# Optimization experiments

Hardware: AMD Instinct MI355X
Metric: run time of the kernel (lower is better)

## Reference

```python
import jax, jax.numpy as jnp
import numpy as np

HIDDEN = 512
INPUT = 128
OUTPUT = 128
PRED_LEN = 32


def _gru_cell(h, gi, gh):
    # gi, gh: [B, 3H] pre-activations (input-side and hidden-side)
    i_r, i_z, i_n = jnp.split(gi, 3, axis=-1)
    h_r, h_z, h_n = jnp.split(gh, 3, axis=-1)
    r = jax.nn.sigmoid(i_r + h_r)
    z = jax.nn.sigmoid(i_z + h_z)
    n = jnp.tanh(i_n + r * h_n)
    return (1.0 - z) * n + z * h


def setup_inputs() -> dict:
    key = jax.random.key(0)
    ks = jax.random.split(key, 7)
    B, L = 512, 512
    s = 0.05
    return {
        "z_seq": jax.random.normal(ks[0], (B, L, INPUT), dtype=jnp.float32),
        "W_ih": jax.random.normal(ks[1], (3 * HIDDEN, INPUT), dtype=jnp.float32) * s,
        "W_hh": jax.random.normal(ks[2], (3 * HIDDEN, HIDDEN), dtype=jnp.float32) * s,
        "b_ih": jax.random.normal(ks[3], (3 * HIDDEN,), dtype=jnp.float32) * s,
        "b_hh": jax.random.normal(ks[4], (3 * HIDDEN,), dtype=jnp.float32) * s,
        "W_out": jax.random.normal(ks[5], (OUTPUT, HIDDEN), dtype=jnp.float32) * s,
        "b_out": jax.random.normal(ks[6], (OUTPUT,), dtype=jnp.float32) * s,
    }


def reference(z_seq, W_ih, W_hh, b_ih, b_hh, W_out, b_out):
    B, L, C = z_seq.shape
    h0 = jnp.zeros((B, HIDDEN), dtype=z_seq.dtype)

    # Precompute input-side pre-activations for all encode steps: [L, B, 3H]
    gi_enc = jnp.einsum('blc,gc->lbg', z_seq, W_ih) + b_ih

    def enc_step(h, gi):
        gh = h @ W_hh.T + b_hh
        return _gru_cell(h, gi, gh), None

    h_t, _ = jax.lax.scan(enc_step, h0, gi_enc)

    # Decode: input is always zeros, so input-side pre-activation is just b_ih
    gi_dec = jnp.broadcast_to(b_ih, (B, 3 * HIDDEN))

    def dec_step(h, _):
        gh = h @ W_hh.T + b_hh
        h_new = _gru_cell(h, gi_dec, gh)
        y = h_new @ W_out.T + b_out
        return h_new, y

    _, ys = jax.lax.scan(dec_step, h_t, None, length=PRED_LEN)  # [pred_len, B, O]
    return jnp.transpose(ys, (1, 0, 2))  # [B, pred_len, O]
```

## Files before the change

kernel.cpp:

```cpp
#include <hip/hip_runtime.h>

#define BATCH 512
#define SEQL  512
#define NIN   128
#define NH    512
#define NOUT  128
#define PRED  32
#define NSTEP (SEQL + PRED)

#define G_B 8
#define G_H 32
#define BT  64
#define NWG (G_B * G_H)
#define NTHREADS 256

#define OFF_WIH  24576
#define OFF_WOUT 30720
#define OFF_TR   38912
#define LDS_SH   40448

typedef short bf16x8 __attribute__((ext_vector_type(8)));
typedef float f32x4 __attribute__((ext_vector_type(4)));
typedef unsigned int u32x4 __attribute__((ext_vector_type(4)));

#define MFMA __builtin_amdgcn_mfma_f32_16x16x32_bf16

__device__ __forceinline__ unsigned short f2bf(float f) {
    unsigned int u = __float_as_uint(f);
    u = (u + 0x7fffu + ((u >> 16) & 1u)) >> 16;
    return (unsigned short)u;
}
__device__ __forceinline__ float sigm(float x) {
    x = fminf(fmaxf(x, -30.f), 30.f);
    return 1.f / (1.f + __expf(-x));
}
__device__ __forceinline__ float tanh_f(float x) {
    x = fminf(fmaxf(x, -15.f), 15.f);
    float e = __expf(2.f * x);
    return (e - 1.f) / (e + 1.f);
}

__global__ __launch_bounds__(256) void zero_kernel(unsigned short* hbuf, int* cnt)
{
    const int tid = threadIdx.x, wg = blockIdx.x;
    u32x4 z = {0, 0, 0, 0};
    char* base = (char*)hbuf + ((wg * 256 + tid) * 32);
    asm volatile("global_store_dwordx4 %0, %1, off sc1" :: "v"(base), "v"(z) : "memory");
    asm volatile("global_store_dwordx4 %0, %1, off offset:16 sc1" :: "v"(base), "v"(z) : "memory");
    if (wg == 0) {
        int zz = 0;
        asm volatile("global_store_dword %0, %1, off sc1" :: "v"(cnt + tid), "v"(zz) : "memory");
        asm volatile("global_store_dword %0, %1, off sc1" :: "v"(cnt + 256 + tid), "v"(zz) : "memory");
        asm volatile("global_store_dword %0, %1, off sc1" :: "v"(cnt + 512 + tid), "v"(zz) : "memory");
        asm volatile("global_store_dword %0, %1, off sc1" :: "v"(cnt + 768 + tid), "v"(zz) : "memory");
    }
}

__global__ __launch_bounds__(NTHREADS, 1) void gru_kernel(
    const float* __restrict__ z_seq, const float* __restrict__ W_ih,
    const float* __restrict__ W_hh, const float* __restrict__ b_ih,
    const float* __restrict__ b_hh, const float* __restrict__ W_out,
    const float* __restrict__ b_out, float* __restrict__ out,
    unsigned short* __restrict__ hbuf, int* __restrict__ cnt)
{
    __shared__ unsigned short s_w[LDS_SH];
    const int tid = threadIdx.x;
    const int wg  = blockIdx.x;
    const int bg  = wg & 7;
    const int hs  = wg >> 3;

    for (int i = tid; i < 24576; i += NTHREADS) {
        int e = i & 7, ln = (i >> 3) & 63, ks = (i >> 9) & 15, g = i >> 13;
        int unit = hs * 16 + (ln & 15);
        int k = ks * 32 + (ln >> 4) * 8 + e;
        s_w[i] = f2bf(W_hh[(g * 512 + unit) * 512 + k]);
    }
    for (int i = tid; i < 6144; i += NTHREADS) {
        int e = i & 7, ln = (i >> 3) & 63, ks = (i >> 9) & 3, g = i >> 11;
        int unit = hs * 16 + (ln & 15);
        int k = ks * 32 + (ln >> 4) * 8 + e;
        s_w[OFF_WIH + i] = f2bf(W_ih[(g * 512 + unit) * 128 + k]);
    }
    for (int i = tid; i < 8192; i += NTHREADS) {
        int e = i & 7, ln = (i >> 3) & 63, ks = i >> 9;
        int ocol = hs * 4 + (ln & 3);
        int k = ks * 32 + (ln >> 4) * 8 + e;
        s_w[OFF_WOUT + i] = f2bf(W_out[ocol * 512 + k]);
    }
    __syncthreads();

    const int lane = tid & 63;
    const int wave = tid >> 6;
    const int li   = lane & 15;
    const int kq   = lane >> 4;
    const int jg   = hs * 16 + li;

    const float bihr = b_ih[jg], bihz = b_ih[NH + jg], bihn = b_ih[2 * NH + jg];
    const float bhhr = b_hh[jg], bhhz = b_hh[NH + jg], bhhn = b_hh[2 * NH + jg];
    const float bo   = b_out[hs * 4 + (li & 3)];

    const int aRow = bg * BT + wave * 16 + li;
    const int cRow = bg * BT + wave * 16 + kq * 4;
    float hreg[4] = {0.f, 0.f, 0.f, 0.f};

    const unsigned short* fb = s_w + lane * 8;
    unsigned short* tr = s_w + OFF_TR + wave * 384;

    int* myFlag = cnt + ((bg * 4 + wave) << 5) + hs;
    const int* fp = cnt + ((bg * 4 + wave) << 5) + (lane & 31);
    int  dead  = 0;

    f32x4 ir = {0,0,0,0}, iz = {0,0,0,0}, in = {0,0,0,0};
    {
        const float* zrow = z_seq + ((long)aRow * SEQL + 0) * NIN + kq * 8;
#pragma unroll
        for (int ks = 0; ks < 4; ++ks) {
            float4 z0 = *(const float4*)(zrow + ks * 32);
            float4 z1 = *(const float4*)(zrow + ks * 32 + 4);
            union { bf16x8 v; unsigned short u[8]; } az;
            az.u[0] = f2bf(z0.x); az.u[1] = f2bf(z0.y);
            az.u[2] = f2bf(z0.z); az.u[3] = f2bf(z0.w);
            az.u[4] = f2bf(z1.x); az.u[5] = f2bf(z1.y);
            az.u[6] = f2bf(z1.z); az.u[7] = f2bf(z1.w);
            ir = MFMA(az.v, *(const bf16x8*)(fb + OFF_WIH + ks * 512), ir, 0, 0, 0);
            iz = MFMA(az.v, *(const bf16x8*)(fb + OFF_WIH + 2048 + ks * 512), iz, 0, 0, 0);
            in = MFMA(az.v, *(const bf16x8*)(fb + OFF_WIH + 4096 + ks * 512), in, 0, 0, 0);
        }
    }

    for (int t = 0; t <= NSTEP; ++t) {
        const unsigned short* hin  = hbuf + (t & 1) * (BATCH * NH);
        unsigned short*       hout = hbuf + ((t & 1) ^ 1) * (BATCH * NH);

        const unsigned short* hrow = hin + aRow * NH + kq * 8;
        bf16x8 a[16];
#pragma unroll
        for (int ks = 0; ks < 16; ++ks)
            asm volatile("global_load_dwordx4 %0, %1, off offset:%2 sc1"
                         : "=v"(a[ks]) : "v"(hrow), "i"(ks * 64) : "memory");
        asm volatile("s_waitcnt vmcnt(0)" ::: "memory");
        __builtin_amdgcn_sched_barrier(0);

        if (t > SEQL) {
            int td = t - SEQL - 1;
            f32x4 y4 = {0, 0, 0, 0};
#pragma unroll
            for (int ks = 0; ks < 16; ++ks)
                y4 = MFMA(a[ks], *(const bf16x8*)(fb + OFF_WOUT + ks * 512), y4, 0, 0, 0);
            if (li < 4) {
#pragma unroll
                for (int q = 0; q < 4; ++q)
                    out[((long)(cRow + q) * PRED + td) * NOUT + hs * 4 + li] = y4[q] + bo;
            }
        }
        if (t == NSTEP) break;

        f32x4 hr = {0,0,0,0}, hz = {0,0,0,0}, hn = {0,0,0,0};
#pragma unroll
        for (int ks = 0; ks < 16; ++ks) {
            hr = MFMA(a[ks], *(const bf16x8*)(fb + ks * 512), hr, 0, 0, 0);
            hz = MFMA(a[ks], *(const bf16x8*)(fb + 8192 + ks * 512), hz, 0, 0, 0);
            hn = MFMA(a[ks], *(const bf16x8*)(fb + 16384 + ks * 512), hn, 0, 0, 0);
        }

#pragma unroll
        for (int q = 0; q < 4; ++q) {
            float r  = sigm(bihr + ir[q] + bhhr + hr[q]);
            float zz = sigm(bihz + iz[q] + bhhz + hz[q]);
            float nn = tanh_f(bihn + in[q] + r * (bhhn + hn[q]));
            float hq = (1.f - zz) * nn + zz * hreg[q];
            hreg[q]  = hq;
            tr[(kq * 4 + q) * 24 + li] = f2bf(hq);
        }
        asm volatile("s_waitcnt lgkmcnt(0)" ::: "memory");
        __builtin_amdgcn_sched_barrier(0);

        if (lane < 32) {
            bf16x8 hv = *(const bf16x8*)(tr + (lane >> 1) * 24 + (lane & 1) * 8);
            int grow = bg * BT + wave * 16 + (lane >> 1);
            unsigned short* hp = hout + grow * NH + hs * 16 + (lane & 1) * 8;
            asm volatile("global_store_dwordx4 %0, %1, off sc1"
                         :: "v"(hp), "v"(hv) : "memory");
        }
        asm volatile("s_waitcnt vmcnt(0)" ::: "memory");
        if (lane == 0) {
            int v = t + 1;
            asm volatile("global_store_dword %0, %1, off sc1"
                         :: "v"(myFlag), "v"(v) : "memory");
        }

        f32x4 nir = {0,0,0,0}, niz = {0,0,0,0}, nin = {0,0,0,0};
        if (t + 1 < SEQL) {
            const float* zrow = z_seq + ((long)aRow * SEQL + (t + 1)) * NIN + kq * 8;
#pragma unroll
            for (int ks = 0; ks < 4; ++ks) {
                float4 z0 = *(const float4*)(zrow + ks * 32);
                float4 z1 = *(const float4*)(zrow + ks * 32 + 4);
                union { bf16x8 v; unsigned short u[8]; } az;
                az.u[0] = f2bf(z0.x); az.u[1] = f2bf(z0.y);
                az.u[2] = f2bf(z0.z); az.u[3] = f2bf(z0.w);
                az.u[4] = f2bf(z1.x); az.u[5] = f2bf(z1.y);
                az.u[6] = f2bf(z1.z); az.u[7] = f2bf(z1.w);
                nir = MFMA(az.v, *(const bf16x8*)(fb + OFF_WIH + ks * 512), nir, 0, 0, 0);
                niz = MFMA(az.v, *(const bf16x8*)(fb + OFF_WIH + 2048 + ks * 512), niz, 0, 0, 0);
                nin = MFMA(az.v, *(const bf16x8*)(fb + OFF_WIH + 4096 + ks * 512), nin, 0, 0, 0);
            }
        }

        const int target = t + 1;
        if (!dead) {
            int patience = 1000000;
            for (;;) {
                int f;
                asm volatile("global_load_dword %0, %1, off sc1\n\ts_waitcnt vmcnt(0)"
                             : "=v"(f) : "v"(fp) : "memory");
                if (__ballot(f >= target) == ~0ull) break;
                if (--patience == 0) { dead = 1; break; }
            }
        }
        __builtin_amdgcn_sched_barrier(0);

        ir = nir; iz = niz; in = nin;
    }
}

extern "C" void kernel_launch(void* const* d_in, const int* in_sizes, int n_in,
                              void* d_out, int out_size, void* d_ws, size_t ws_size,
                              hipStream_t stream)
{
    const float* z_seq = (const float*)d_in[0];
    const float* W_ih  = (const float*)d_in[1];
    const float* W_hh  = (const float*)d_in[2];
    const float* b_ih  = (const float*)d_in[3];
    const float* b_hh  = (const float*)d_in[4];
    const float* W_out = (const float*)d_in[5];
    const float* b_out = (const float*)d_in[6];
    float* out = (float*)d_out;

    unsigned short* hbuf = (unsigned short*)d_ws;
    int* cnt = (int*)((char*)d_ws + (size_t)2 * BATCH * NH * 2);

    zero_kernel<<<dim3(64), dim3(256), 0, stream>>>(hbuf, cnt);
    gru_kernel<<<dim3(NWG), dim3(NTHREADS), 0, stream>>>(
        z_seq, W_ih, W_hh, b_ih, b_hh, W_out, b_out, out, hbuf, cnt);
}
```

Measured before the change: 3.204 ms.

## Add runtime-verified fast sync path with non-sc1 h loads and per-WG flags

Replaces the per-wave flag barrier with one flag per workgroup (after a __syncthreads), polled by a single lane that reads a whole row of flags with vector loads. At startup it checks that all workgroups of a batch group sit on the same XCD and runs a coherence probe. If both checks pass, a fast path loads h and polls flags without sc1, using buffer_inv instead. It also skips the h load at t=0 and shrinks the zero kernel. The aim is to cut the cross-workgroup synchronisation and coherent-load latency that dominates each recurrent step. The cost is a fragile startup handshake, and correctness depends on the XCD placement check.

```diff
diff --git a/kernel.cpp b/kernel.cpp
--- a/kernel.cpp
+++ b/kernel.cpp
@@ -19,11 +19,20 @@
 #define OFF_TR   38912
 #define LDS_SH   40448
 
+#define SLOW_FLAG_OFF 1048576
+#define XCD_OFF       1052672
+#define CANT_OFF      1053696
+#define CANC_OFF      1054720
+#define FAST_FLAG_OFF 1056768
+#define WS_NEED       1058816
+
 typedef short bf16x8 __attribute__((ext_vector_type(8)));
 typedef float f32x4 __attribute__((ext_vector_type(4)));
 typedef unsigned int u32x4 __attribute__((ext_vector_type(4)));
 
 #define MFMA __builtin_amdgcn_mfma_f32_16x16x32_bf16
+
+template<bool B> struct BC { static constexpr bool value = B; };
 
 __device__ __forceinline__ unsigned short f2bf(float f) {
     unsigned int u = __float_as_uint(f);
@@ -39,20 +48,62 @@
     float e = __expf(2.f * x);
     return (e - 1.f) / (e + 1.f);
 }
-
-__global__ __launch_bounds__(256) void zero_kernel(unsigned short* hbuf, int* cnt)
+__device__ __forceinline__ int poll_word_sc1(const int* p) {
+    int v;
+    asm volatile("global_load_dword %0, %1, off sc1\n\ts_waitcnt vmcnt(0)"
+                 : "=v"(v) : "v"(p) : "memory");
+    return v;
+}
+
+#define POLL_ROW_BODY(PREFIX, SCBITS)                                      \
+    int4 f0, f1, f2, f3, f4, f5, f6, f7;                                   \
+    asm volatile(                                                          \
+        PREFIX                                                             \
+        "global_load_dwordx4 %0, %8, off " SCBITS "\n\t"                   \
+        "global_load_dwordx4 %1, %8, off offset:16 " SCBITS "\n\t"         \
+        "global_load_dwordx4 %2, %8, off offset:32 " SCBITS "\n\t"         \
+        "global_load_dwordx4 %3, %8, off offset:48 " SCBITS "\n\t"         \
+        "global_load_dwordx4 %4, %8, off offset:64 " SCBITS "\n\t"         \
+        "global_load_dwordx4 %5, %8, off offset:80 " SCBITS "\n\t"         \
+        "global_load_dwordx4 %6, %8, off offset:96 " SCBITS "\n\t"         \
+        "global_load_dwordx4 %7, %8, off offset:112 " SCBITS "\n\t"        \
+        "s_waitcnt vmcnt(0)"                                               \
+        : "=&v"(f0), "=&v"(f1), "=&v"(f2), "=&v"(f3),                      \
+          "=&v"(f4), "=&v"(f5), "=&v"(f6), "=&v"(f7)                       \
+        : "v"(p) : "memory");                                              \
+    int mn = min(min(min(min(f0.x, f0.y), min(f0.z, f0.w)),                \
+                     min(min(f1.x, f1.y), min(f1.z, f1.w))),               \
+                 min(min(min(f2.x, f2.y), min(f2.z, f2.w)),                \
+                     min(min(f3.x, f3.y), min(f3.z, f3.w))));              \
+    mn = min(mn, min(min(min(min(f4.x, f4.y), min(f4.z, f4.w)),            \
+                         min(min(f5.x, f5.y), min(f5.z, f5.w))),           \
+                     min(min(min(f6.x, f6.y), min(f6.z, f6.w)),            \
+                         min(min(f7.x, f7.y), min(f7.z, f7.w)))));         \
+    int mx = max(max(max(max(f0.x, f0.y), max(f0.z, f0.w)),                \
+                     max(max(f1.x, f1.y), max(f1.z, f1.w))),               \
+                 max(max(max(f2.x, f2.y), max(f2.z, f2.w)),                \
+                     max(max(f3.x, f3.y), max(f3.z, f3.w))));              \
+    mx = max(mx, max(max(max(max(f4.x, f4.y), max(f4.z, f4.w)),            \
+                         max(max(f5.x, f5.y), max(f5.z, f5.w))),           \
+                     max(max(max(f6.x, f6.y), max(f6.z, f6.w)),            \
+                         max(max(f7.x, f7.y), max(f7.z, f7.w)))));         \
+    return make_int2(mn, mx);
+
+__device__ __forceinline__ int2 poll_row_sc1(const int* p) { POLL_ROW_BODY("", "sc1") }
+__device__ __forceinline__ int2 poll_row_inv(const int* p) {
+    POLL_ROW_BODY("buffer_inv\n\ts_waitcnt vmcnt(0)\n\t", "")
+}
+
+__global__ __launch_bounds__(256) void zero_kernel(char* ws)
 {
     const int tid = threadIdx.x, wg = blockIdx.x;
     u32x4 z = {0, 0, 0, 0};
-    char* base = (char*)hbuf + ((wg * 256 + tid) * 32);
-    asm volatile("global_store_dwordx4 %0, %1, off sc1" :: "v"(base), "v"(z) : "memory");
-    asm volatile("global_store_dwordx4 %0, %1, off offset:16 sc1" :: "v"(base), "v"(z) : "memory");
     if (wg == 0) {
-        int zz = 0;
-        asm volatile("global_store_dword %0, %1, off sc1" :: "v"(cnt + tid), "v"(zz) : "memory");
-        asm volatile("global_store_dword %0, %1, off sc1" :: "v"(cnt + 256 + tid), "v"(zz) : "memory");
-        asm volatile("global_store_dword %0, %1, off sc1" :: "v"(cnt + 512 + tid), "v"(zz) : "memory");
-        asm volatile("global_store_dword %0, %1, off sc1" :: "v"(cnt + 768 + tid), "v"(zz) : "memory");
+        char* p = ws + SLOW_FLAG_OFF + tid * 16;
+        asm volatile("global_store_dwordx4 %0, %1, off sc1" :: "v"(p), "v"(z) : "memory");
+    } else if (tid < 192) {
+        char* p = ws + XCD_OFF + tid * 16;
+        asm volatile("global_store_dwordx4 %0, %1, off sc1" :: "v"(p), "v"(z) : "memory");
     }
 }
 
@@ -61,13 +112,21 @@
     const float* __restrict__ W_hh, const float* __restrict__ b_ih,
     const float* __restrict__ b_hh, const float* __restrict__ W_out,
     const float* __restrict__ b_out, float* __restrict__ out,
-    unsigned short* __restrict__ hbuf, int* __restrict__ cnt)
+    char* __restrict__ ws, int allow_fast)
 {
     __shared__ unsigned short s_w[LDS_SH];
+    __shared__ int s_fast;
     const int tid = threadIdx.x;
     const int wg  = blockIdx.x;
     const int bg  = wg & 7;
     const int hs  = wg >> 3;
+
+    unsigned short* hbuf = (unsigned short*)ws;
+    int* sfl  = (int*)(ws + SLOW_FLAG_OFF) + bg * 64;
+    int* ffl  = (int*)(ws + FAST_FLAG_OFF) + bg * 64;
+    int* xrow = (int*)(ws + XCD_OFF)  + bg * 32;
+    int* T    = (int*)(ws + CANT_OFF) + bg * 32;
+    int* C    = (int*)(ws + CANC_OFF) + bg * 32;
 
     for (int i = tid; i < 24576; i += NTHREADS) {
         int e = i & 7, ln = (i >> 3) & 63, ks = (i >> 9) & 15, g = i >> 13;
@@ -87,7 +146,69 @@
         int k = ks * 32 + (ln >> 4) * 8 + e;
         s_w[OFF_WOUT + i] = f2bf(W_out[ocol * 512 + k]);
     }
+
+    unsigned xcd;
+    asm volatile("s_getreg_b32 %0, hwreg(20, 0, 32)" : "=s"(xcd));
+    xcd &= 255u;
+    if (tid == 0) {
+        int z0 = 0;
+        asm volatile("global_store_dword %0, %1, off sc1" :: "v"(ffl + hs), "v"(z0) : "memory");
+        asm volatile("s_waitcnt vmcnt(0)" ::: "memory");
+        int xv = (int)xcd + 1;
+        asm volatile("global_store_dword %0, %1, off sc1" :: "v"(xrow + hs), "v"(xv) : "memory");
+
+        if (hs == 0) {
+            unsigned long long tm;
+            asm volatile("s_memtime %0" : "=s"(tm));
+            int m1 = (int)((unsigned)tm | 1u);
+            asm volatile("global_store_dword %0, %1, off sc1" :: "v"(T), "v"(m1) : "memory");
+            asm volatile("s_waitcnt vmcnt(0)" ::: "memory");
+            asm volatile("global_store_dword %0, %1, off sc1" :: "v"(C), "v"(m1) : "memory");
+            int p = 1000000;
+            while (poll_word_sc1(C + 1) == 0 && --p) {}
+            if (p) {
+                int m2 = m1 ^ 0x5A5A5A5A;
+                asm volatile("global_store_dword %0, %1, off sc1" :: "v"(T), "v"(m2) : "memory");
+                asm volatile("s_waitcnt vmcnt(0)" ::: "memory");
+                int one = 1;
+                asm volatile("global_store_dword %0, %1, off sc1" :: "v"(C + 2), "v"(one) : "memory");
+            }
+        } else if (hs == 1) {
+            int p = 1000000, m1;
+            while ((m1 = poll_word_sc1(C)) == 0 && --p) {}
+            int verdict = 1;
+            if (p) {
+                int pv;
+                asm volatile("global_load_dword %0, %1, off\n\ts_waitcnt vmcnt(0)"
+                             : "=v"(pv) : "v"(T) : "memory");
+                asm volatile("" :: "v"(pv));
+                int one = 1;
+                asm volatile("global_store_dword %0, %1, off sc1" :: "v"(C + 1), "v"(one) : "memory");
+                int q = 1000000;
+                while (poll_word_sc1(C + 2) == 0 && --q) {}
+                if (q) {
+                    int v2;
+                    asm volatile("buffer_inv\n\ts_waitcnt vmcnt(0)\n\t"
+                                 "global_load_dword %0, %1, off\n\ts_waitcnt vmcnt(0)"
+                                 : "=v"(v2) : "v"(T) : "memory");
+                    verdict = (v2 == (m1 ^ 0x5A5A5A5A)) ? 2 : 1;
+                }
+            }
+            asm volatile("global_store_dword %0, %1, off sc1" :: "v"(C + 3), "v"(verdict) : "memory");
+        }
+
+        int ok = 0, p2 = 1000000;
+        for (;;) {
+            int2 mm = poll_row_sc1(xrow);
+            if (mm.x > 0) { ok = (mm.x == mm.y); break; }
+            if (--p2 == 0) break;
+        }
+        int vd = 0, p3 = 1000000;
+        while ((vd = poll_word_sc1(C + 3)) == 0 && --p3) {}
+        s_fast = (allow_fast && ok && vd == 2) ? 1 : 0;
+    }
     __syncthreads();
+    const bool fast = (s_fast != 0);
 
     const int lane = tid & 63;
     const int wave = tid >> 6;
@@ -105,10 +226,7 @@
 
     const unsigned short* fb = s_w + lane * 8;
     unsigned short* tr = s_w + OFF_TR + wave * 384;
-
-    int* myFlag = cnt + ((bg * 4 + wave) << 5) + hs;
-    const int* fp = cnt + ((bg * 4 + wave) << 5) + (lane & 31);
-    int  dead  = 0;
+    int dead = 0;
 
     f32x4 ir = {0,0,0,0}, iz = {0,0,0,0}, in = {0,0,0,0};
     {
@@ -128,100 +246,121 @@
         }
     }
 
-    for (int t = 0; t <= NSTEP; ++t) {
-        const unsigned short* hin  = hbuf + (t & 1) * (BATCH * NH);
-        unsigned short*       hout = hbuf + ((t & 1) ^ 1) * (BATCH * NH);
-
-        const unsigned short* hrow = hin + aRow * NH + kq * 8;
-        bf16x8 a[16];
-#pragma unroll
-        for (int ks = 0; ks < 16; ++ks)
-            asm volatile("global_load_dwordx4 %0, %1, off offset:%2 sc1"
-                         : "=v"(a[ks]) : "v"(hrow), "i"(ks * 64) : "memory");
-        asm volatile("s_waitcnt vmcnt(0)" ::: "memory");
-        __builtin_amdgcn_sched_barrier(0);
-
-        if (t > SEQL) {
-            int td = t - SEQL - 1;
-            f32x4 y4 = {0, 0, 0, 0};
-#pragma unroll
-            for (int ks = 0; ks < 16; ++ks)
-                y4 = MFMA(a[ks], *(const bf16x8*)(fb + OFF_WOUT + ks * 512), y4, 0, 0, 0);
-            if (li < 4) {
-#pragma unroll
-                for (int q = 0; q < 4; ++q)
-                    out[((long)(cRow + q) * PRED + td) * NOUT + hs * 4 + li] = y4[q] + bo;
-            }
+    auto body = [&](auto FC) {
+        constexpr bool FAST = decltype(FC)::value;
+        for (int t = 0; t <= NSTEP; ++t) {
+            const unsigned short* hin  = hbuf + (t & 1) * (BATCH * NH);
+            unsigned short*       hout = hbuf + ((t & 1) ^ 1) * (BATCH * NH);
+
+            bf16x8 a[16];
+            if (t == 0) {
+                bf16x8 az = {0,0,0,0,0,0,0,0};
+#pragma unroll
+                for (int ks = 0; ks < 16; ++ks) a[ks] = az;
+            } else {
+                const unsigned short* hrow = hin + aRow * NH + kq * 8;
+#pragma unroll
+                for (int ks = 0; ks < 16; ++ks) {
+                    if constexpr (FAST)
+                        asm volatile("global_load_dwordx4 %0, %1, off offset:%2"
+                                     : "=v"(a[ks]) : "v"(hrow), "i"(ks * 64) : "memory");
+                    else
+                        asm volatile("global_load_dwordx4 %0, %1, off offset:%2 sc1"
+                                     : "=v"(a[ks]) : "v"(hrow), "i"(ks * 64) : "memory");
+                }
+                asm volatile("s_waitcnt vmcnt(0)" ::: "memory");
+                __builtin_amdgcn_sched_barrier(0);
+            }
+
+            if (t > SEQL) {
+                int td = t - SEQL - 1;
+                f32x4 y4 = {0, 0, 0, 0};
+#pragma unroll
+                for (int ks = 0; ks < 16; ++ks)
+                    y4 = MFMA(a[ks], *(const bf16x8*)(fb + OFF_WOUT + ks * 512), y4, 0, 0, 0);
+                if (li < 4) {
+#pragma unroll
+                    for (int q = 0; q < 4; ++q)
+                        out[((long)(cRow + q) * PRED + td) * NOUT + hs * 4 + li] = y4[q] + bo;
+                }
+            }
+            if (t == NSTEP) break;
+
+            f32x4 hr = {0,0,0,0}, hz = {0,0,0,0}, hn = {0,0,0,0};
+#pragma unroll
+            for (int ks = 0; ks < 16; ++ks) {
+                hr = MFMA(a[ks], *(const bf16x8*)(fb + ks * 512), hr, 0, 0, 0);
+                hz = MFMA(a[ks], *(const bf16x8*)(fb + 8192 + ks * 512), hz, 0, 0, 0);
+                hn = MFMA(a[ks], *(const bf16x8*)(fb + 16384 + ks * 512), hn, 0, 0, 0);
+            }
+
+#pragma unroll
+            for (int q = 0; q < 4; ++q) {
+                float r  = sigm(bihr + ir[q] + bhhr + hr[q]);
+                float zz = sigm(bihz + iz[q] + bhhz + hz[q]);
+                float nn = tanh_f(bihn + in[q] + r * (bhhn + hn[q]));
+                float hq = (1.f - zz) * nn + zz * hreg[q];
+                hreg[q]  = hq;
+                tr[(kq * 4 + q) * 24 + li] = f2bf(hq);
+            }
+            asm volatile("s_waitcnt lgkmcnt(0)" ::: "memory");
+            __builtin_amdgcn_sched_barrier(0);
+
+            if (lane < 32) {
+                bf16x8 hv = *(const bf16x8*)(tr + (lane >> 1) * 24 + (lane & 1) * 8);
+                int grow = bg * BT + wave * 16 + (lane >> 1);
+                unsigned short* hp = hout + grow * NH + hs * 16 + (lane & 1) * 8;
+                asm volatile("global_store_dwordx4 %0, %1, off sc1"
+                             :: "v"(hp), "v"(hv) : "memory");
+            }
+            asm volatile("s_waitcnt vmcnt(0)" ::: "memory");
+            __syncthreads();
+            if (tid == 0) {
+                int v = t + 1;
+                asm volatile("global_store_dword %0, %1, off sc1"
+                             :: "v"(sfl + hs), "v"(v) : "memory");
+                asm volatile("global_store_dword %0, %1, off sc1"
+                             :: "v"(ffl + hs), "v"(v) : "memory");
+            }
+
+            f32x4 nir = {0,0,0,0}, niz = {0,0,0,0}, nin = {0,0,0,0};
+            if (t + 1 < SEQL) {
+                const float* zrow = z_seq + ((long)aRow * SEQL + (t + 1)) * NIN + kq * 8;
+#pragma unroll
+                for (int ks = 0; ks < 4; ++ks) {
+                    float4 z0 = *(const float4*)(zrow + ks * 32);
+                    float4 z1 = *(const float4*)(zrow + ks * 32 + 4);
+                    union { bf16x8 v; unsigned short u[8]; } az;
+                    az.u[0] = f2bf(z0.x); az.u[1] = f2bf(z0.y);
+                    az.u[2] = f2bf(z0.z); az.u[3] = f2bf(z0.w);
+                    az.u[4] = f2bf(z1.x); az.u[5] = f2bf(z1.y);
+                    az.u[6] = f2bf(z1.z); az.u[7] = f2bf(z1.w);
+                    nir = MFMA(az.v, *(const bf16x8*)(fb + OFF_WIH + ks * 512), nir, 0, 0, 0);
+                    niz = MFMA(az.v, *(const bf16x8*)(fb + OFF_WIH + 2048 + ks * 512), niz, 0, 0, 0);
+                    nin = MFMA(az.v, *(const bf16x8*)(fb + OFF_WIH + 4096 + ks * 512), nin, 0, 0, 0);
+                }
+            }
+
+            const int target = t + 1;
+            int bail = 0;
+            if (!dead && lane == 0) {
+                int patience = 1000000;
+                for (;;) {
+                    int2 mm;
+                    if constexpr (FAST) mm = poll_row_inv(ffl);
+                    else                mm = poll_row_sc1(sfl);
+                    if (mm.x >= target) break;
+                    if (--patience == 0) { bail = 1; break; }
+                }
+            }
+            dead |= __builtin_amdgcn_readfirstlane(bail);
+            __builtin_amdgcn_sched_barrier(0);
+
+            ir = nir; iz = niz; in = nin;
         }
-        if (t == NSTEP) break;
-
-        f32x4 hr = {0,0,0,0}, hz = {0,0,0,0}, hn = {0,0,0,0};
-#pragma unroll
-        for (int ks = 0; ks < 16; ++ks) {
-            hr = MFMA(a[ks], *(const bf16x8*)(fb + ks * 512), hr, 0, 0, 0);
-            hz = MFMA(a[ks], *(const bf16x8*)(fb + 8192 + ks * 512), hz, 0, 0, 0);
-            hn = MFMA(a[ks], *(const bf16x8*)(fb + 16384 + ks * 512), hn, 0, 0, 0);
-        }
-
-#pragma unroll
-        for (int q = 0; q < 4; ++q) {
-            float r  = sigm(bihr + ir[q] + bhhr + hr[q]);
-            float zz = sigm(bihz + iz[q] + bhhz + hz[q]);
-            float nn = tanh_f(bihn + in[q] + r * (bhhn + hn[q]));
-            float hq = (1.f - zz) * nn + zz * hreg[q];
-            hreg[q]  = hq;
-            tr[(kq * 4 + q) * 24 + li] = f2bf(hq);
-        }
-        asm volatile("s_waitcnt lgkmcnt(0)" ::: "memory");
-        __builtin_amdgcn_sched_barrier(0);
-
-        if (lane < 32) {
-            bf16x8 hv = *(const bf16x8*)(tr + (lane >> 1) * 24 + (lane & 1) * 8);
-            int grow = bg * BT + wave * 16 + (lane >> 1);
-            unsigned short* hp = hout + grow * NH + hs * 16 + (lane & 1) * 8;
-            asm volatile("global_store_dwordx4 %0, %1, off sc1"
-                         :: "v"(hp), "v"(hv) : "memory");
-        }
-        asm volatile("s_waitcnt vmcnt(0)" ::: "memory");
-        if (lane == 0) {
-            int v = t + 1;
-            asm volatile("global_store_dword %0, %1, off sc1"
-                         :: "v"(myFlag), "v"(v) : "memory");
-        }
-
-        f32x4 nir = {0,0,0,0}, niz = {0,0,0,0}, nin = {0,0,0,0};
-        if (t + 1 < SEQL) {
-            const float* zrow = z_seq + ((long)aRow * SEQL + (t + 1)) * NIN + kq * 8;
-#pragma unroll
-            for (int ks = 0; ks < 4; ++ks) {
-                float4 z0 = *(const float4*)(zrow + ks * 32);
-                float4 z1 = *(const float4*)(zrow + ks * 32 + 4);
-                union { bf16x8 v; unsigned short u[8]; } az;
-                az.u[0] = f2bf(z0.x); az.u[1] = f2bf(z0.y);
-                az.u[2] = f2bf(z0.z); az.u[3] = f2bf(z0.w);
-                az.u[4] = f2bf(z1.x); az.u[5] = f2bf(z1.y);
-                az.u[6] = f2bf(z1.z); az.u[7] = f2bf(z1.w);
-                nir = MFMA(az.v, *(const bf16x8*)(fb + OFF_WIH + ks * 512), nir, 0, 0, 0);
-                niz = MFMA(az.v, *(const bf16x8*)(fb + OFF_WIH + 2048 + ks * 512), niz, 0, 0, 0);
-                nin = MFMA(az.v, *(const bf16x8*)(fb + OFF_WIH + 4096 + ks * 512), nin, 0, 0, 0);
-            }
-        }
-
-        const int target = t + 1;
-        if (!dead) {
-            int patience = 1000000;
-            for (;;) {
-                int f;
-                asm volatile("global_load_dword %0, %1, off sc1\n\ts_waitcnt vmcnt(0)"
-                             : "=v"(f) : "v"(fp) : "memory");
-                if (__ballot(f >= target) == ~0ull) break;
-                if (--patience == 0) { dead = 1; break; }
-            }
-        }
-        __builtin_amdgcn_sched_barrier(0);
-
-        ir = nir; iz = niz; in = nin;
-    }
+    };
+    if (fast) body(BC<true>{});
+    else      body(BC<false>{});
 }
 
 extern "C" void kernel_launch(void* const* d_in, const int* in_sizes, int n_in,
@@ -237,10 +376,10 @@
     const float* b_out = (const float*)d_in[6];
     float* out = (float*)d_out;
 
-    unsigned short* hbuf = (unsigned short*)d_ws;
-    int* cnt = (int*)((char*)d_ws + (size_t)2 * BATCH * NH * 2);
-
-    zero_kernel<<<dim3(64), dim3(256), 0, stream>>>(hbuf, cnt);
+    int allow_fast = (ws_size >= (size_t)WS_NEED) ? 1 : 0;
+
+    zero_kernel<<<dim3(2), dim3(256), 0, stream>>>((char*)d_ws);
     gru_kernel<<<dim3(NWG), dim3(NTHREADS), 0, stream>>>(
-        z_seq, W_ih, W_hh, b_ih, b_hh, W_out, b_out, out, hbuf, cnt);
-}
+        z_seq, W_ih, W_hh, b_ih, b_hh, W_out, b_out, out,
+        (char*)d_ws, allow_fast);
+}
```

New measurement: 2.770 ms. -13.5%, faster.
